# Performance work log

Hardware: AMD Instinct MI355X
Metric: run time of the kernel (lower is better)

The kernel has to match this reference:

```python
import jax, jax.numpy as jnp
import numpy as np

B, IN_CH, OUT_CH, K, H, W = 1, 64, 64, 4, 512, 512
N = H * W  # per-pixel sampling: one point per output pixel


def setup_inputs() -> dict:
    key = jax.random.key(0)
    ks = jax.random.split(key, 9)
    inp = {
        "input": jax.random.normal(ks[0], (B, IN_CH, H, W), dtype=jnp.float32),
        "ax": jax.random.uniform(ks[1], (B, N), dtype=jnp.float32) * (W - 1),
        "ay": jax.random.uniform(ks[2], (B, N), dtype=jnp.float32) * (H - 1),
        # 1x1 conv params (kernel is [out,in] since kh=kw=1)
        "conv_w": jax.random.normal(ks[3], (OUT_CH, IN_CH), dtype=jnp.float32) * 0.05,
        "conv_b": jax.random.normal(ks[4], (OUT_CH,), dtype=jnp.float32) * 0.05,
        "offset_w": jax.random.normal(ks[5], (K, 2, IN_CH), dtype=jnp.float32) * 0.05,
        "offset_b": jax.random.normal(ks[6], (K, 2), dtype=jnp.float32) * 0.05,
        "wconv_w": jax.random.normal(ks[7], (K, IN_CH), dtype=jnp.float32) * 0.05,
        "wconv_b": jax.random.normal(ks[8], (K,), dtype=jnp.float32) * 0.05,
    }
    return inp


def _bilinear(feat, xs, ys):
    """feat [C,H,W]; xs, ys [m] pixel coords; bilinear, zero padding. -> [C,m]."""
    C, Hh, Ww = feat.shape
    x0f = jnp.floor(xs)
    y0f = jnp.floor(ys)
    wx = xs - x0f
    wy = ys - y0f
    x0 = x0f.astype(jnp.int32)
    y0 = y0f.astype(jnp.int32)
    out = jnp.zeros((C, xs.shape[0]), dtype=feat.dtype)
    corners = ((0, 0, (1 - wx) * (1 - wy)), (1, 0, wx * (1 - wy)),
               (0, 1, (1 - wx) * wy), (1, 1, wx * wy))
    for dx, dy, wgt in corners:
        xc = x0 + dx
        yc = y0 + dy
        valid = (xc >= 0) & (xc < Ww) & (yc >= 0) & (yc < Hh)
        v = feat[:, jnp.clip(yc, 0, Hh - 1), jnp.clip(xc, 0, Ww - 1)]  # [C,m]
        out = out + v * (wgt * valid)[None, :]
    return out


def reference(input, ax, ay, conv_w, conv_b, offset_w, offset_b, wconv_w, wconv_b):
    b, c, h, w = input.shape
    k = offset_w.shape[0]
    n = ax.shape[1]  # == h*w
    # 1x1 convs as einsums
    proj = jnp.einsum('bchw,oc->bohw', input, conv_w) + conv_b[None, :, None, None]
    flows = jnp.einsum('bchw,kdc->bkdhw', input, offset_w) + offset_b[None, :, :, None, None]  # [b,k,2,h,w]
    weights = jax.nn.softmax(
        jnp.einsum('bchw,kc->bkhw', input, wconv_w) + wconv_b[None, :, None, None], axis=1)  # [b,k,h,w]
    # gather flow at truncated integer coords (flow[num, iy, ix, :])
    ix = jnp.trunc(ax).astype(jnp.int32)  # [b,n]
    iy = jnp.trunc(ay).astype(jnp.int32)
    flow_pts = jax.vmap(lambda fl, i, j: fl[:, :, j, i])(flows, ix, iy)  # [b,k,2,n]
    vx = ax[:, None, :] + flow_pts[:, :, 0]  # [b,k,n]
    vy = ay[:, None, :] + flow_pts[:, :, 1]
    # torch normalizes align_corners=True-style then grid_sample (align_corners=False) unnormalizes:
    # pixel = v * W/(W-1) - 0.5
    xs = vx * (w / (w - 1)) - 0.5
    ys = vy * (h / (h - 1)) - 0.5
    samp = jax.vmap(lambda f, x, y: _bilinear(f, x.reshape(-1), y.reshape(-1)))(proj, xs, ys)  # [b,C,k*n]
    feats = samp.reshape(b, proj.shape[1], k, h, w).transpose(0, 2, 1, 3, 4)  # [b,k,C,h,w]
    return (weights[:, :, None, :, :] * feats).sum(axis=1)  # [b,out_ch,h,w]
```

## Files before the change

kernel.cpp:

```cpp
#include <hip/hip_runtime.h>
#include <hip/hip_bf16.h>

#define NPIX (512 * 512)
#define IMW 512
#define IMH 512

typedef float fvec4 __attribute__((ext_vector_type(4)));

static __device__ __forceinline__ unsigned short f2bf(float f) {
  union { __hip_bfloat16 h; unsigned short u; } cv;
  cv.h = __float2bfloat16(f);
  return cv.u;
}

static __device__ __forceinline__ unsigned pack2bf(float lo, float hi) {
  return (unsigned)f2bf(lo) | ((unsigned)f2bf(hi) << 16);
}

__global__ __launch_bounds__(256) void k1_pointwise(
    const float* __restrict__ in, const float* __restrict__ conv_w,
    const float* __restrict__ conv_b, const float* __restrict__ offset_w,
    const float* __restrict__ offset_b, const float* __restrict__ wconv_w,
    const float* __restrict__ wconv_b, __hip_bfloat16* __restrict__ proj_t,
    float* __restrict__ flows_t, float* __restrict__ wts_t) {
  const int n = blockIdx.x * 256 + threadIdx.x;

#pragma unroll 1
  for (int half = 0; half < 2; ++half) {
    const float* wbase = conv_w + half * 32 * 64;
    const float* bbase = conv_b + half * 32;
    float acc[32];
#pragma unroll
    for (int o = 0; o < 32; ++o) acc[o] = bbase[o];
#pragma unroll 1
    for (int cb = 0; cb < 64; cb += 8) {
      float x[8];
#pragma unroll
      for (int j = 0; j < 8; ++j) x[j] = in[(size_t)(cb + j) * NPIX + n];
#pragma unroll
      for (int o = 0; o < 32; ++o) {
#pragma unroll
        for (int j = 0; j < 8; ++j)
          acc[o] = fmaf(x[j], wbase[o * 64 + cb + j], acc[o]);
      }
    }
    uint4* pj = (uint4*)(proj_t + (size_t)n * 64 + half * 32);
    uint4 v0, v1, v2, v3;
    v0.x = pack2bf(acc[0], acc[1]);   v0.y = pack2bf(acc[2], acc[3]);
    v0.z = pack2bf(acc[4], acc[5]);   v0.w = pack2bf(acc[6], acc[7]);
    v1.x = pack2bf(acc[8], acc[9]);   v1.y = pack2bf(acc[10], acc[11]);
    v1.z = pack2bf(acc[12], acc[13]); v1.w = pack2bf(acc[14], acc[15]);
    v2.x = pack2bf(acc[16], acc[17]); v2.y = pack2bf(acc[18], acc[19]);
    v2.z = pack2bf(acc[20], acc[21]); v2.w = pack2bf(acc[22], acc[23]);
    v3.x = pack2bf(acc[24], acc[25]); v3.y = pack2bf(acc[26], acc[27]);
    v3.z = pack2bf(acc[28], acc[29]); v3.w = pack2bf(acc[30], acc[31]);
    pj[0] = v0; pj[1] = v1; pj[2] = v2; pj[3] = v3;
  }

  {
    float acc[12];
#pragma unroll
    for (int o = 0; o < 8; ++o) acc[o] = offset_b[o];
#pragma unroll
    for (int o = 0; o < 4; ++o) acc[8 + o] = wconv_b[o];
#pragma unroll 1
    for (int cb = 0; cb < 64; cb += 8) {
      float x[8];
#pragma unroll
      for (int j = 0; j < 8; ++j) x[j] = in[(size_t)(cb + j) * NPIX + n];
#pragma unroll
      for (int o = 0; o < 8; ++o) {
#pragma unroll
        for (int j = 0; j < 8; ++j)
          acc[o] = fmaf(x[j], offset_w[o * 64 + cb + j], acc[o]);
      }
#pragma unroll
      for (int o = 0; o < 4; ++o) {
#pragma unroll
        for (int j = 0; j < 8; ++j)
          acc[8 + o] = fmaf(x[j], wconv_w[o * 64 + cb + j], acc[8 + o]);
      }
    }
    float4* fl4 = (float4*)(flows_t + (size_t)n * 8);
    fl4[0] = make_float4(acc[0], acc[1], acc[2], acc[3]);
    fl4[1] = make_float4(acc[4], acc[5], acc[6], acc[7]);

    const float m = fmaxf(fmaxf(acc[8], acc[9]), fmaxf(acc[10], acc[11]));
    const float e0 = __expf(acc[8] - m), e1 = __expf(acc[9] - m);
    const float e2 = __expf(acc[10] - m), e3 = __expf(acc[11] - m);
    const float inv = 1.f / (e0 + e1 + e2 + e3);
    *(float4*)(wts_t + (size_t)n * 4) =
        make_float4(e0 * inv, e1 * inv, e2 * inv, e3 * inv);
  }
}

static __device__ __forceinline__ void sample_one(
    float axv, float ayv, float4 f01, float4 f23, float4 wk4,
    const __hip_bfloat16* __restrict__ proj_t, int l8,
    float* __restrict__ dst) {
  const float fx[4] = {f01.x, f01.z, f23.x, f23.z};
  const float fy[4] = {f01.y, f01.w, f23.y, f23.w};
  const float wk[4] = {wk4.x, wk4.y, wk4.z, wk4.w};

  float acc[8];
#pragma unroll
  for (int j = 0; j < 8; ++j) acc[j] = 0.f;

#pragma unroll
  for (int k = 0; k < 4; ++k) {
    const float xs = (axv + fx[k]) * (512.f / 511.f) - 0.5f;
    const float ys = (ayv + fy[k]) * (512.f / 511.f) - 0.5f;
    const float x0f = floorf(xs), y0f = floorf(ys);
    const float wx = xs - x0f, wy = ys - y0f;
    const int x0 = (int)x0f, y0 = (int)y0f;
    const int x1 = x0 + 1, y1 = y0 + 1;
    const int cx0 = min(max(x0, 0), IMW - 1);
    const int cx1 = min(max(x1, 0), IMW - 1);
    const int cy0 = min(max(y0, 0), IMH - 1);
    const int cy1 = min(max(y1, 0), IMH - 1);
    const float vx0 = (x0 >= 0 && x0 < IMW) ? 1.f : 0.f;
    const float vx1 = (x1 >= 0 && x1 < IMW) ? 1.f : 0.f;
    const float vy0 = (y0 >= 0 && y0 < IMH) ? 1.f : 0.f;
    const float vy1 = (y1 >= 0 && y1 < IMH) ? 1.f : 0.f;
    const float s00 = wk[k] * (1.f - wx) * (1.f - wy) * vx0 * vy0;
    const float s10 = wk[k] * wx * (1.f - wy) * vx1 * vy0;
    const float s01 = wk[k] * (1.f - wx) * wy * vx0 * vy1;
    const float s11 = wk[k] * wx * wy * vx1 * vy1;

    const uint4 u00 = *(const uint4*)(proj_t + (size_t)(cy0 * IMW + cx0) * 64 + l8 * 8);
    const uint4 u10 = *(const uint4*)(proj_t + (size_t)(cy0 * IMW + cx1) * 64 + l8 * 8);
    const uint4 u01 = *(const uint4*)(proj_t + (size_t)(cy1 * IMW + cx0) * 64 + l8 * 8);
    const uint4 u11 = *(const uint4*)(proj_t + (size_t)(cy1 * IMW + cx1) * 64 + l8 * 8);

    const unsigned w00[4] = {u00.x, u00.y, u00.z, u00.w};
    const unsigned w10[4] = {u10.x, u10.y, u10.z, u10.w};
    const unsigned w01[4] = {u01.x, u01.y, u01.z, u01.w};
    const unsigned w11[4] = {u11.x, u11.y, u11.z, u11.w};
#pragma unroll
    for (int q = 0; q < 4; ++q) {
      acc[2 * q] = fmaf(__uint_as_float(w00[q] << 16), s00, acc[2 * q]);
      acc[2 * q] = fmaf(__uint_as_float(w10[q] << 16), s10, acc[2 * q]);
      acc[2 * q] = fmaf(__uint_as_float(w01[q] << 16), s01, acc[2 * q]);
      acc[2 * q] = fmaf(__uint_as_float(w11[q] << 16), s11, acc[2 * q]);
      acc[2 * q + 1] = fmaf(__uint_as_float(w00[q] & 0xffff0000u), s00, acc[2 * q + 1]);
      acc[2 * q + 1] = fmaf(__uint_as_float(w10[q] & 0xffff0000u), s10, acc[2 * q + 1]);
      acc[2 * q + 1] = fmaf(__uint_as_float(w01[q] & 0xffff0000u), s01, acc[2 * q + 1]);
      acc[2 * q + 1] = fmaf(__uint_as_float(w11[q] & 0xffff0000u), s11, acc[2 * q + 1]);
    }
  }
  *(float4*)(dst) = make_float4(acc[0], acc[1], acc[2], acc[3]);
  *(float4*)(dst + 4) = make_float4(acc[4], acc[5], acc[6], acc[7]);
}

__global__ __launch_bounds__(256) void k2_sample(
    const float* __restrict__ ax, const float* __restrict__ ay,
    const __hip_bfloat16* __restrict__ proj_t,
    const float* __restrict__ flows_t, const float* __restrict__ wts_t,
    float* __restrict__ out) {
  __shared__ float tile[64][68];
  const int t = threadIdx.x;
  const int g8 = t >> 3;
  const int l8 = t & 7;
  const int p0 = blockIdx.x * 64;
  const int pA = p0 + g8;
  const int pB = p0 + 32 + g8;

  const float axA = ax[pA], ayA = ay[pA];
  const float axB = ax[pB], ayB = ay[pB];
  const float4 wkA = *(const float4*)(wts_t + (size_t)pA * 4);
  const float4 wkB = *(const float4*)(wts_t + (size_t)pB * 4);
  const size_t nA = (size_t)((int)ayA * IMW + (int)axA);
  const size_t nB = (size_t)((int)ayB * IMW + (int)axB);
  const float4 fA01 = *(const float4*)(flows_t + nA * 8);
  const float4 fA23 = *(const float4*)(flows_t + nA * 8 + 4);
  const float4 fB01 = *(const float4*)(flows_t + nB * 8);
  const float4 fB23 = *(const float4*)(flows_t + nB * 8 + 4);

  sample_one(axA, ayA, fA01, fA23, wkA, proj_t, l8, &tile[g8][8 * l8]);
  sample_one(axB, ayB, fB01, fB23, wkB, proj_t, l8, &tile[32 + g8][8 * l8]);
  __syncthreads();

  const int g16 = t >> 4;
  const int l16 = t & 15;
#pragma unroll
  for (int it = 0; it < 4; ++it) {
    const int c = it * 16 + g16;
    fvec4 vv;
    vv.x = tile[4 * l16 + 0][c];
    vv.y = tile[4 * l16 + 1][c];
    vv.z = tile[4 * l16 + 2][c];
    vv.w = tile[4 * l16 + 3][c];
    __builtin_nontemporal_store(
        vv, (fvec4*)(out + (size_t)c * NPIX + p0 + 4 * l16));
  }
}

extern "C" void kernel_launch(void* const* d_in, const int* in_sizes, int n_in,
                              void* d_out, int out_size, void* d_ws,
                              size_t ws_size, hipStream_t stream) {
  const float* input = (const float*)d_in[0];
  const float* ax = (const float*)d_in[1];
  const float* ay = (const float*)d_in[2];
  const float* conv_w = (const float*)d_in[3];
  const float* conv_b = (const float*)d_in[4];
  const float* offset_w = (const float*)d_in[5];
  const float* offset_b = (const float*)d_in[6];
  const float* wconv_w = (const float*)d_in[7];
  const float* wconv_b = (const float*)d_in[8];
  float* out = (float*)d_out;

  __hip_bfloat16* proj_t = (__hip_bfloat16*)d_ws;
  float* flows_t = (float*)(proj_t + (size_t)NPIX * 64);
  float* wts_t = flows_t + (size_t)NPIX * 8;

  hipLaunchKernelGGL(k1_pointwise, dim3(NPIX / 256), dim3(256), 0, stream,
                     input, conv_w, conv_b, offset_w, offset_b, wconv_w,
                     wconv_b, proj_t, flows_t, wts_t);
  hipLaunchKernelGGL(k2_sample, dim3(NPIX / 64), dim3(256), 0, stream, ax, ay,
                     proj_t, flows_t, wts_t, out);
}
```

Before: 247.6 us.

## Bin sample points spatially, split pointwise conv roles, store flows and outputs in bf16

Sample points are counting-sorted into 64 spatial bins (hist, scan, scatter kernels), so each sampling block gathers from a compact image region and gets better L2 locality. The sampler writes a bf16 point-major intermediate, and a separate transpose kernel produces the channel-major fp32 output. The pointwise kernel now uses 320 threads, each computing 16 projection channels or the flow/weight heads, and stores flows as bf16. This adds four kernel launches, a memset and an extra round trip through the bf16 intermediate, and bf16 flows and outputs cost some precision.

```diff
diff --git a/kernel.cpp b/kernel.cpp
--- a/kernel.cpp
+++ b/kernel.cpp
@@ -4,6 +4,7 @@
 #define NPIX (512 * 512)
 #define IMW 512
 #define IMH 512
+#define NBINS 64
 
 typedef float fvec4 __attribute__((ext_vector_type(4)));
 
@@ -12,52 +13,52 @@
   cv.h = __float2bfloat16(f);
   return cv.u;
 }
-
 static __device__ __forceinline__ unsigned pack2bf(float lo, float hi) {
   return (unsigned)f2bf(lo) | ((unsigned)f2bf(hi) << 16);
 }
-
-__global__ __launch_bounds__(256) void k1_pointwise(
+static __device__ __forceinline__ float bflo(unsigned u) {
+  return __uint_as_float(u << 16);
+}
+static __device__ __forceinline__ float bfhi(unsigned u) {
+  return __uint_as_float(u & 0xffff0000u);
+}
+
+__global__ __launch_bounds__(320) void k1_pointwise(
     const float* __restrict__ in, const float* __restrict__ conv_w,
     const float* __restrict__ conv_b, const float* __restrict__ offset_w,
     const float* __restrict__ offset_b, const float* __restrict__ wconv_w,
     const float* __restrict__ wconv_b, __hip_bfloat16* __restrict__ proj_t,
-    float* __restrict__ flows_t, float* __restrict__ wts_t) {
-  const int n = blockIdx.x * 256 + threadIdx.x;
-
-#pragma unroll 1
-  for (int half = 0; half < 2; ++half) {
-    const float* wbase = conv_w + half * 32 * 64;
-    const float* bbase = conv_b + half * 32;
-    float acc[32];
-#pragma unroll
-    for (int o = 0; o < 32; ++o) acc[o] = bbase[o];
+    __hip_bfloat16* __restrict__ flows_t, float* __restrict__ wts_t) {
+  const int role = threadIdx.x >> 6;
+  const int n = blockIdx.x * 64 + (threadIdx.x & 63);
+
+  if (role < 4) {
+    const float* wbase = conv_w + role * 16 * 64;
+    const float* bbase = conv_b + role * 16;
+    float acc[16];
+#pragma unroll
+    for (int o = 0; o < 16; ++o) acc[o] = bbase[o];
 #pragma unroll 1
     for (int cb = 0; cb < 64; cb += 8) {
       float x[8];
 #pragma unroll
       for (int j = 0; j < 8; ++j) x[j] = in[(size_t)(cb + j) * NPIX + n];
 #pragma unroll
-      for (int o = 0; o < 32; ++o) {
+      for (int o = 0; o < 16; ++o) {
 #pragma unroll
         for (int j = 0; j < 8; ++j)
           acc[o] = fmaf(x[j], wbase[o * 64 + cb + j], acc[o]);
       }
     }
-    uint4* pj = (uint4*)(proj_t + (size_t)n * 64 + half * 32);
-    uint4 v0, v1, v2, v3;
+    uint4 v0, v1;
     v0.x = pack2bf(acc[0], acc[1]);   v0.y = pack2bf(acc[2], acc[3]);
     v0.z = pack2bf(acc[4], acc[5]);   v0.w = pack2bf(acc[6], acc[7]);
     v1.x = pack2bf(acc[8], acc[9]);   v1.y = pack2bf(acc[10], acc[11]);
     v1.z = pack2bf(acc[12], acc[13]); v1.w = pack2bf(acc[14], acc[15]);
-    v2.x = pack2bf(acc[16], acc[17]); v2.y = pack2bf(acc[18], acc[19]);
-    v2.z = pack2bf(acc[20], acc[21]); v2.w = pack2bf(acc[22], acc[23]);
-    v3.x = pack2bf(acc[24], acc[25]); v3.y = pack2bf(acc[26], acc[27]);
-    v3.z = pack2bf(acc[28], acc[29]); v3.w = pack2bf(acc[30], acc[31]);
-    pj[0] = v0; pj[1] = v1; pj[2] = v2; pj[3] = v3;
-  }
-
-  {
+    uint4* pj = (uint4*)(proj_t + (size_t)n * 64 + role * 16);
+    pj[0] = v0;
+    pj[1] = v1;
+  } else {
     float acc[12];
 #pragma unroll
     for (int o = 0; o < 8; ++o) acc[o] = offset_b[o];
@@ -81,9 +82,12 @@
           acc[8 + o] = fmaf(x[j], wconv_w[o * 64 + cb + j], acc[8 + o]);
       }
     }
-    float4* fl4 = (float4*)(flows_t + (size_t)n * 8);
-    fl4[0] = make_float4(acc[0], acc[1], acc[2], acc[3]);
-    fl4[1] = make_float4(acc[4], acc[5], acc[6], acc[7]);
+    uint4 fv;
+    fv.x = pack2bf(acc[0], acc[1]);
+    fv.y = pack2bf(acc[2], acc[3]);
+    fv.z = pack2bf(acc[4], acc[5]);
+    fv.w = pack2bf(acc[6], acc[7]);
+    *(uint4*)(flows_t + (size_t)n * 8) = fv;
 
     const float m = fmaxf(fmaxf(acc[8], acc[9]), fmaxf(acc[10], acc[11]));
     const float e0 = __expf(acc[8] - m), e1 = __expf(acc[9] - m);
@@ -94,94 +98,147 @@
   }
 }
 
-static __device__ __forceinline__ void sample_one(
-    float axv, float ayv, float4 f01, float4 f23, float4 wk4,
-    const __hip_bfloat16* __restrict__ proj_t, int l8,
-    float* __restrict__ dst) {
-  const float fx[4] = {f01.x, f01.z, f23.x, f23.z};
-  const float fy[4] = {f01.y, f01.w, f23.y, f23.w};
-  const float wk[4] = {wk4.x, wk4.y, wk4.z, wk4.w};
-
-  float acc[8];
-#pragma unroll
-  for (int j = 0; j < 8; ++j) acc[j] = 0.f;
-
-#pragma unroll
-  for (int k = 0; k < 4; ++k) {
-    const float xs = (axv + fx[k]) * (512.f / 511.f) - 0.5f;
-    const float ys = (ayv + fy[k]) * (512.f / 511.f) - 0.5f;
-    const float x0f = floorf(xs), y0f = floorf(ys);
-    const float wx = xs - x0f, wy = ys - y0f;
-    const int x0 = (int)x0f, y0 = (int)y0f;
-    const int x1 = x0 + 1, y1 = y0 + 1;
-    const int cx0 = min(max(x0, 0), IMW - 1);
-    const int cx1 = min(max(x1, 0), IMW - 1);
-    const int cy0 = min(max(y0, 0), IMH - 1);
-    const int cy1 = min(max(y1, 0), IMH - 1);
-    const float vx0 = (x0 >= 0 && x0 < IMW) ? 1.f : 0.f;
-    const float vx1 = (x1 >= 0 && x1 < IMW) ? 1.f : 0.f;
-    const float vy0 = (y0 >= 0 && y0 < IMH) ? 1.f : 0.f;
-    const float vy1 = (y1 >= 0 && y1 < IMH) ? 1.f : 0.f;
-    const float s00 = wk[k] * (1.f - wx) * (1.f - wy) * vx0 * vy0;
-    const float s10 = wk[k] * wx * (1.f - wy) * vx1 * vy0;
-    const float s01 = wk[k] * (1.f - wx) * wy * vx0 * vy1;
-    const float s11 = wk[k] * wx * wy * vx1 * vy1;
-
-    const uint4 u00 = *(const uint4*)(proj_t + (size_t)(cy0 * IMW + cx0) * 64 + l8 * 8);
-    const uint4 u10 = *(const uint4*)(proj_t + (size_t)(cy0 * IMW + cx1) * 64 + l8 * 8);
-    const uint4 u01 = *(const uint4*)(proj_t + (size_t)(cy1 * IMW + cx0) * 64 + l8 * 8);
-    const uint4 u11 = *(const uint4*)(proj_t + (size_t)(cy1 * IMW + cx1) * 64 + l8 * 8);
-
-    const unsigned w00[4] = {u00.x, u00.y, u00.z, u00.w};
-    const unsigned w10[4] = {u10.x, u10.y, u10.z, u10.w};
-    const unsigned w01[4] = {u01.x, u01.y, u01.z, u01.w};
-    const unsigned w11[4] = {u11.x, u11.y, u11.z, u11.w};
-#pragma unroll
-    for (int q = 0; q < 4; ++q) {
-      acc[2 * q] = fmaf(__uint_as_float(w00[q] << 16), s00, acc[2 * q]);
-      acc[2 * q] = fmaf(__uint_as_float(w10[q] << 16), s10, acc[2 * q]);
-      acc[2 * q] = fmaf(__uint_as_float(w01[q] << 16), s01, acc[2 * q]);
-      acc[2 * q] = fmaf(__uint_as_float(w11[q] << 16), s11, acc[2 * q]);
-      acc[2 * q + 1] = fmaf(__uint_as_float(w00[q] & 0xffff0000u), s00, acc[2 * q + 1]);
-      acc[2 * q + 1] = fmaf(__uint_as_float(w10[q] & 0xffff0000u), s10, acc[2 * q + 1]);
-      acc[2 * q + 1] = fmaf(__uint_as_float(w01[q] & 0xffff0000u), s01, acc[2 * q + 1]);
-      acc[2 * q + 1] = fmaf(__uint_as_float(w11[q] & 0xffff0000u), s11, acc[2 * q + 1]);
-    }
-  }
-  *(float4*)(dst) = make_float4(acc[0], acc[1], acc[2], acc[3]);
-  *(float4*)(dst + 4) = make_float4(acc[4], acc[5], acc[6], acc[7]);
-}
-
-__global__ __launch_bounds__(256) void k2_sample(
+static __device__ __forceinline__ int bin_of(float axv, float ayv) {
+  const int ix = (int)axv, iy = (int)ayv;
+  return ((iy >> 6) << 3) | (ix >> 6);
+}
+
+__global__ __launch_bounds__(256) void k2a_hist(const float* __restrict__ ax,
+                                                const float* __restrict__ ay,
+                                                int* __restrict__ hist) {
+  __shared__ int h[NBINS];
+  const int t = threadIdx.x;
+  if (t < NBINS) h[t] = 0;
+  __syncthreads();
+  const int p = blockIdx.x * 256 + t;
+  atomicAdd(&h[bin_of(ax[p], ay[p])], 1);
+  __syncthreads();
+  if (t < NBINS && h[t] > 0) atomicAdd(&hist[t], h[t]);
+}
+
+__global__ void k2b_scan(const int* __restrict__ hist,
+                         int* __restrict__ cursor) {
+  if (threadIdx.x == 0) {
+    int run = 0;
+    for (int b = 0; b < NBINS; ++b) {
+      cursor[b] = run;
+      run += hist[b];
+    }
+  }
+}
+
+__global__ __launch_bounds__(256) void k2c_scatter(
+    const float* __restrict__ ax, const float* __restrict__ ay,
+    int* __restrict__ cursor, int* __restrict__ order) {
+  __shared__ int h[NBINS], base[NBINS], off[NBINS];
+  const int t = threadIdx.x;
+  if (t < NBINS) { h[t] = 0; off[t] = 0; }
+  __syncthreads();
+  const int p = blockIdx.x * 256 + t;
+  const int b = bin_of(ax[p], ay[p]);
+  atomicAdd(&h[b], 1);
+  __syncthreads();
+  if (t < NBINS && h[t] > 0) base[t] = atomicAdd(&cursor[t], h[t]);
+  __syncthreads();
+  const int r = atomicAdd(&off[b], 1);
+  order[base[b] + r] = p;
+}
+
+__global__ __launch_bounds__(256) void k2d_sample(
     const float* __restrict__ ax, const float* __restrict__ ay,
     const __hip_bfloat16* __restrict__ proj_t,
-    const float* __restrict__ flows_t, const float* __restrict__ wts_t,
-    float* __restrict__ out) {
+    const __hip_bfloat16* __restrict__ flows_t,
+    const float* __restrict__ wts_t, const int* __restrict__ order,
+    __hip_bfloat16* __restrict__ outp) {
+  const int t = threadIdx.x;
+  const int g8 = t >> 3, l8 = t & 7;
+  const int bid = blockIdx.x;
+  const int chunk = (bid & 7) * (NPIX / 64 / 8) + (bid >> 3);
+
+#pragma unroll 1
+  for (int pass = 0; pass < 2; ++pass) {
+    const int pid = order[chunk * 64 + pass * 32 + g8];
+    const float axv = ax[pid], ayv = ay[pid];
+    const float4 wk4 = *(const float4*)(wts_t + (size_t)pid * 4);
+    const size_t n2 = (size_t)((int)ayv * IMW + (int)axv);
+    const uint4 fw = *(const uint4*)(flows_t + n2 * 8);
+    const float fx[4] = {bflo(fw.x), bflo(fw.y), bflo(fw.z), bflo(fw.w)};
+    const float fy[4] = {bfhi(fw.x), bfhi(fw.y), bfhi(fw.z), bfhi(fw.w)};
+    const float wk[4] = {wk4.x, wk4.y, wk4.z, wk4.w};
+
+    float acc[8];
+#pragma unroll
+    for (int j = 0; j < 8; ++j) acc[j] = 0.f;
+
+#pragma unroll
+    for (int k = 0; k < 4; ++k) {
+      const float xs = (axv + fx[k]) * (512.f / 511.f) - 0.5f;
+      const float ys = (ayv + fy[k]) * (512.f / 511.f) - 0.5f;
+      const float x0f = floorf(xs), y0f = floorf(ys);
+      const float wx = xs - x0f, wy = ys - y0f;
+      const int x0 = (int)x0f, y0 = (int)y0f;
+      const int x1 = x0 + 1, y1 = y0 + 1;
+      const int cx0 = min(max(x0, 0), IMW - 1);
+      const int cx1 = min(max(x1, 0), IMW - 1);
+      const int cy0 = min(max(y0, 0), IMH - 1);
+      const int cy1 = min(max(y1, 0), IMH - 1);
+      const float vx0 = (x0 >= 0 && x0 < IMW) ? 1.f : 0.f;
+      const float vx1 = (x1 >= 0 && x1 < IMW) ? 1.f : 0.f;
+      const float vy0 = (y0 >= 0 && y0 < IMH) ? 1.f : 0.f;
+      const float vy1 = (y1 >= 0 && y1 < IMH) ? 1.f : 0.f;
+      const float s00 = wk[k] * (1.f - wx) * (1.f - wy) * vx0 * vy0;
+      const float s10 = wk[k] * wx * (1.f - wy) * vx1 * vy0;
+      const float s01 = wk[k] * (1.f - wx) * wy * vx0 * vy1;
+      const float s11 = wk[k] * wx * wy * vx1 * vy1;
+
+      const uint4 u00 = *(const uint4*)(proj_t + (size_t)(cy0 * IMW + cx0) * 64 + l8 * 8);
+      const uint4 u10 = *(const uint4*)(proj_t + (size_t)(cy0 * IMW + cx1) * 64 + l8 * 8);
+      const uint4 u01 = *(const uint4*)(proj_t + (size_t)(cy1 * IMW + cx0) * 64 + l8 * 8);
+      const uint4 u11 = *(const uint4*)(proj_t + (size_t)(cy1 * IMW + cx1) * 64 + l8 * 8);
+
+      const unsigned w00[4] = {u00.x, u00.y, u00.z, u00.w};
+      const unsigned w10[4] = {u10.x, u10.y, u10.z, u10.w};
+      const unsigned w01[4] = {u01.x, u01.y, u01.z, u01.w};
+      const unsigned w11[4] = {u11.x, u11.y, u11.z, u11.w};
+#pragma unroll
+      for (int q = 0; q < 4; ++q) {
+        acc[2 * q] = fmaf(bflo(w00[q]), s00, acc[2 * q]);
+        acc[2 * q] = fmaf(bflo(w10[q]), s10, acc[2 * q]);
+        acc[2 * q] = fmaf(bflo(w01[q]), s01, acc[2 * q]);
+        acc[2 * q] = fmaf(bflo(w11[q]), s11, acc[2 * q]);
+        acc[2 * q + 1] = fmaf(bfhi(w00[q]), s00, acc[2 * q + 1]);
+        acc[2 * q + 1] = fmaf(bfhi(w10[q]), s10, acc[2 * q + 1]);
+        acc[2 * q + 1] = fmaf(bfhi(w01[q]), s01, acc[2 * q + 1]);
+        acc[2 * q + 1] = fmaf(bfhi(w11[q]), s11, acc[2 * q + 1]);
+      }
+    }
+    uint4 o;
+    o.x = pack2bf(acc[0], acc[1]);
+    o.y = pack2bf(acc[2], acc[3]);
+    o.z = pack2bf(acc[4], acc[5]);
+    o.w = pack2bf(acc[6], acc[7]);
+    *(uint4*)(outp + (size_t)pid * 64 + l8 * 8) = o;
+  }
+}
+
+__global__ __launch_bounds__(256) void k3_transpose(
+    const __hip_bfloat16* __restrict__ outp, float* __restrict__ out) {
   __shared__ float tile[64][68];
   const int t = threadIdx.x;
-  const int g8 = t >> 3;
-  const int l8 = t & 7;
+  const int g8 = t >> 3, l8 = t & 7;
   const int p0 = blockIdx.x * 64;
-  const int pA = p0 + g8;
-  const int pB = p0 + 32 + g8;
-
-  const float axA = ax[pA], ayA = ay[pA];
-  const float axB = ax[pB], ayB = ay[pB];
-  const float4 wkA = *(const float4*)(wts_t + (size_t)pA * 4);
-  const float4 wkB = *(const float4*)(wts_t + (size_t)pB * 4);
-  const size_t nA = (size_t)((int)ayA * IMW + (int)axA);
-  const size_t nB = (size_t)((int)ayB * IMW + (int)axB);
-  const float4 fA01 = *(const float4*)(flows_t + nA * 8);
-  const float4 fA23 = *(const float4*)(flows_t + nA * 8 + 4);
-  const float4 fB01 = *(const float4*)(flows_t + nB * 8);
-  const float4 fB23 = *(const float4*)(flows_t + nB * 8 + 4);
-
-  sample_one(axA, ayA, fA01, fA23, wkA, proj_t, l8, &tile[g8][8 * l8]);
-  sample_one(axB, ayB, fB01, fB23, wkB, proj_t, l8, &tile[32 + g8][8 * l8]);
-  __syncthreads();
-
-  const int g16 = t >> 4;
-  const int l16 = t & 15;
+#pragma unroll
+  for (int pass = 0; pass < 2; ++pass) {
+    const int pl = pass * 32 + g8;
+    const uint4 u = *(const uint4*)(outp + (size_t)(p0 + pl) * 64 + l8 * 8);
+    float* dst = &tile[pl][8 * l8];
+    dst[0] = bflo(u.x); dst[1] = bfhi(u.x);
+    dst[2] = bflo(u.y); dst[3] = bfhi(u.y);
+    dst[4] = bflo(u.z); dst[5] = bfhi(u.z);
+    dst[6] = bflo(u.w); dst[7] = bfhi(u.w);
+  }
+  __syncthreads();
+  const int g16 = t >> 4, l16 = t & 15;
 #pragma unroll
   for (int it = 0; it < 4; ++it) {
     const int c = it * 16 + g16;
@@ -210,12 +267,24 @@
   float* out = (float*)d_out;
 
   __hip_bfloat16* proj_t = (__hip_bfloat16*)d_ws;
-  float* flows_t = (float*)(proj_t + (size_t)NPIX * 64);
-  float* wts_t = flows_t + (size_t)NPIX * 8;
-
-  hipLaunchKernelGGL(k1_pointwise, dim3(NPIX / 256), dim3(256), 0, stream,
+  __hip_bfloat16* outp = proj_t + (size_t)NPIX * 64;
+  __hip_bfloat16* flows_t = outp + (size_t)NPIX * 64;
+  float* wts_t = (float*)(flows_t + (size_t)NPIX * 8);
+  int* order = (int*)(wts_t + (size_t)NPIX * 4);
+  int* hist = order + NPIX;
+  int* cursor = hist + NBINS;
+
+  hipMemsetAsync(hist, 0, 2 * NBINS * sizeof(int), stream);
+  hipLaunchKernelGGL(k1_pointwise, dim3(NPIX / 64), dim3(320), 0, stream,
                      input, conv_w, conv_b, offset_w, offset_b, wconv_w,
                      wconv_b, proj_t, flows_t, wts_t);
-  hipLaunchKernelGGL(k2_sample, dim3(NPIX / 64), dim3(256), 0, stream, ax, ay,
-                     proj_t, flows_t, wts_t, out);
-}
+  hipLaunchKernelGGL(k2a_hist, dim3(NPIX / 256), dim3(256), 0, stream, ax, ay,
+                     hist);
+  hipLaunchKernelGGL(k2b_scan, dim3(1), dim3(64), 0, stream, hist, cursor);
+  hipLaunchKernelGGL(k2c_scatter, dim3(NPIX / 256), dim3(256), 0, stream, ax,
+                     ay, cursor, order);
+  hipLaunchKernelGGL(k2d_sample, dim3(NPIX / 64), dim3(256), 0, stream, ax, ay,
+                     proj_t, flows_t, wts_t, order, outp);
+  hipLaunchKernelGGL(k3_transpose, dim3(NPIX / 64), dim3(256), 0, stream, outp,
+                     out);
+}
```

After: 369.1 us. 49.1% more time.
